# Optimization experiments

Hardware: AMD Instinct MI355X
Metric: run time of the kernel (lower is better)

Reference implementation:

```python
import jax, jax.numpy as jnp
import numpy as np

Q = 4096  # num_quantizing
E = 256   # quantizing_dim


def setup_inputs() -> dict:
    key = jax.random.key(0)
    kx, kw = jax.random.split(key)
    x = jax.random.normal(kx, (16, 2048, E), dtype=jnp.float32)
    # nn.init.normal_(weight, mean=0.0, std=0.001)
    weight = 0.001 * jax.random.normal(kw, (Q, E), dtype=jnp.float32)
    return {"x": x, "weight": weight}


def reference(x, weight):
    # x: (*, E), weight: (Q, E)
    input_shape = x.shape
    xf = x.reshape(-1, weight.shape[1])  # (N, E)
    # Squared L2 distance via norm expansion (same argmin as sum(delta^2)):
    x2 = jnp.sum(xf * xf, axis=1, keepdims=True)          # (N, 1)
    w2 = jnp.sum(weight * weight, axis=1)                  # (Q,)
    dist = x2 - 2.0 * (xf @ weight.T) + w2                 # (N, Q)
    q_idx = jnp.argmin(dist, axis=1)                       # (N,)
    q_data = weight[q_idx]                                 # (N, E)
    return q_data.reshape(input_shape), q_idx.reshape(input_shape[:-1])
```

## Files before the change

### kernel.cpp

```cpp
#include <hip/hip_runtime.h>
#include <cfloat>
#include <climits>

constexpr int E  = 256;
constexpr int Qn = 4096;
constexpr float WSCALE = 4096.0f;


typedef _Float16 half8  __attribute__((ext_vector_type(8)));
typedef _Float16 half4v __attribute__((ext_vector_type(4)));
typedef float    f32x16 __attribute__((ext_vector_type(16)));

#define GAS __attribute__((address_space(1)))
#define LAS __attribute__((address_space(3)))

#define NEG_INF __int_as_float(0xFF800000)

__device__ inline bool lexlt(float a, int ai, float b, int bi) {
    return a < b || (a == b && ai < bi);
}

__global__ __launch_bounds__(256) void prep_kernel(
    const float* __restrict__ x, const float* __restrict__ w,
    _Float16* __restrict__ A16, _Float16* __restrict__ B16,
    float* __restrict__ w2, int nxblocks)
{
    int blk  = blockIdx.x;
    int sub  = threadIdx.x >> 6;
    int lane = threadIdx.x & 63;
    bool isX = blk < nxblocks;
    int row  = (isX ? blk : blk - nxblocks) * 4 + sub;

    const float* src = isX ? x : w;
    float4 v = *(const float4*)(src + (size_t)row * E + lane * 4);

    if (!isX) {
        float s = v.x * v.x + v.y * v.y + v.z * v.z + v.w * v.w;
        #pragma unroll
        for (int off = 32; off; off >>= 1) s += __shfl_xor(s, off);
        if (lane == 0) w2[row] = s;
    }

    float sc = isX ? 1.0f : WSCALE;
    half4v h = { (_Float16)(v.x * sc), (_Float16)(v.y * sc),
                 (_Float16)(v.z * sc), (_Float16)(v.w * sc) };
    _Float16* dst16 = (isX ? A16 : B16) + (size_t)row * 256;
    *(half4v*)(dst16 + lane * 4) = h;
}

__device__ inline void ins4max(float K[4], float k) {
    #pragma unroll
    for (int t = 0; t < 4; ++t) {
        float mx = fmaxf(K[t], k);
        k = fminf(K[t], k);
        K[t] = mx;
    }
}

union SmemU {
    struct { _Float16 W[128 * 64]; _Float16 X[128 * 64]; } st;
    float2 mergeS[128 * 4];
};

__global__ __launch_bounds__(256, 4) void vq_mfma_kernel(
    const _Float16* __restrict__ A16,
    const _Float16* __restrict__ B16,
    float4* __restrict__ top4)
{
    __shared__ SmemU sm;

    const int tid  = threadIdx.x;
    const int w    = tid >> 6;
    const int lane = tid & 63;
    const int l31  = lane & 31;
    const int lh   = lane >> 5;
    const int rb   = blockIdx.x;
    const int cg   = blockIdx.y;

    const int wr = (w & 1) * 64;
    const int wc = (w >> 1) * 64;

    f32x16 acc[2][2];
    #pragma unroll
    for (int f = 0; f < 2; ++f)
        #pragma unroll
        for (int g = 0; g < 2; ++g)
            #pragma unroll
            for (int r = 0; r < 16; ++r) acc[f][g][r] = 0.0f;

    const _Float16* Ab16 = A16 + (size_t)rb * 128 * 256;
    const _Float16* Bb16 = B16 + (size_t)cg * 128 * 256;

    const int srow = lane >> 3;
    const int schk = lane & 7;

    for (int kt = 0; kt < 4; ++kt) {
        __syncthreads();
        #pragma unroll
        for (int inst = 0; inst < 4; ++inst) {
            int drow = w * 32 + inst * 8 + srow;
            int gchk = schk ^ (drow & 7);
            const _Float16* gW = Bb16 + (size_t)drow * 256 + kt * 64 + gchk * 8;
            const _Float16* gX = Ab16 + (size_t)drow * 256 + kt * 64 + gchk * 8;
            __builtin_amdgcn_global_load_lds((const GAS void*)gW,
                (LAS void*)(sm.st.W + w * 2048 + inst * 512), 16, 0, 0);
            __builtin_amdgcn_global_load_lds((const GAS void*)gX,
                (LAS void*)(sm.st.X + w * 2048 + inst * 512), 16, 0, 0);
        }
        __syncthreads();

        #pragma unroll
        for (int s = 0; s < 4; ++s) {
            const int kc = 2 * s + lh;
            half8 wf[2], xf[2];
            #pragma unroll
            for (int f = 0; f < 2; ++f) {
                int fr = wc + 32 * f + l31;
                wf[f] = *(const half8*)(sm.st.W + fr * 64 + ((kc ^ (fr & 7)) << 3));
                int xr = wr + 32 * f + l31;
                xf[f] = *(const half8*)(sm.st.X + xr * 64 + ((kc ^ (xr & 7)) << 3));
            }
            #pragma unroll
            for (int f = 0; f < 2; ++f)
                #pragma unroll
                for (int g = 0; g < 2; ++g)
                    acc[f][g] = __builtin_amdgcn_mfma_f32_32x32x16_f16(
                        wf[f], xf[g], acc[f][g], 0, 0, 0);
        }
    }

    float t1[2] = { NEG_INF, NEG_INF }, t2[2] = { NEG_INF, NEG_INF };

    #pragma unroll
    for (int f = 0; f < 2; ++f)
        #pragma unroll
        for (int r = 0; r < 16; ++r) {
            int m  = (r & 3) + 8 * (r >> 2) + 4 * lh;
            int qg = cg * 128 + wc + 32 * f + m;
            #pragma unroll
            for (int g = 0; g < 2; ++g) {
                float pk = __int_as_float(
                    (__float_as_int(acc[f][g][r]) & 0xFFFFF000) | qg);
                t2[g] = __builtin_amdgcn_fmed3f(t1[g], t2[g], pk);
                t1[g] = fmaxf(t1[g], pk);
            }
        }

    __syncthreads();

    #pragma unroll
    for (int g = 0; g < 2; ++g) {
        int rrow = wr + 32 * g + l31;
        sm.mergeS[rrow * 4 + ((w >> 1) * 2 + lh)] = make_float2(t1[g], t2[g]);
    }
    __syncthreads();

    if (tid < 128) {
        float K[4] = { NEG_INF, NEG_INF, NEG_INF, NEG_INF };
        #pragma unroll
        for (int sl = 0; sl < 4; ++sl) {
            float2 a = sm.mergeS[tid * 4 + sl];
            ins4max(K, a.x);
            ins4max(K, a.y);
        }
        top4[(size_t)(rb * 128 + tid) * 32 + cg] =
            make_float4(K[0], K[1], K[2], K[3]);
    }
}

__global__ __launch_bounds__(256) void finalize_kernel(
    const float4* __restrict__ top4, const float* __restrict__ x,
    const float* __restrict__ w, const float* __restrict__ w2,
    float* __restrict__ qdata, float* __restrict__ qidx)
{
    int row  = blockIdx.x * 4 + (threadIdx.x >> 6);
    int lane = threadIdx.x & 63;

    float cand[4];
    if (lane < 32) {
        float4 c4 = top4[(size_t)row * 32 + lane];
        cand[0] = c4.x; cand[1] = c4.y; cand[2] = c4.z; cand[3] = c4.w;
    } else {
        cand[0] = cand[1] = cand[2] = cand[3] = NEG_INF;
    }

    int chosen[4];
    #pragma unroll
    for (int p = 0; p < 4; ++p) {
        float cur = fmaxf(fmaxf(cand[0], cand[1]), fmaxf(cand[2], cand[3]));
        #pragma unroll
        for (int off = 32; off; off >>= 1)
            cur = fmaxf(cur, __shfl_xor(cur, off));
        int curb = __float_as_int(cur);
        chosen[p] = curb & 0xFFF;
        #pragma unroll
        for (int j = 0; j < 4; ++j)
            if (__float_as_int(cand[j]) == curb) cand[j] = NEG_INF;
    }

    float4 xv = *(const float4*)(x + (size_t)row * E + lane * 4);
    float s2 = xv.x * xv.x + xv.y * xv.y + xv.z * xv.z + xv.w * xv.w;
    float d[4];
    #pragma unroll
    for (int j = 0; j < 4; ++j) {
        float4 wv = *(const float4*)(w + (size_t)chosen[j] * E + lane * 4);
        d[j] = xv.x * wv.x + xv.y * wv.y + xv.z * wv.z + xv.w * wv.w;
    }
    #pragma unroll
    for (int off = 32; off; off >>= 1) {
        s2 += __shfl_xor(s2, off);
        #pragma unroll
        for (int j = 0; j < 4; ++j) d[j] += __shfl_xor(d[j], off);
    }

    float bs = FLT_MAX; int win = INT_MAX;
    #pragma unroll
    for (int j = 0; j < 4; ++j) {
        float s = (s2 - 2.0f * d[j]) + w2[chosen[j]];
        if (lexlt(s, chosen[j], bs, win)) { bs = s; win = chosen[j]; }
    }

    if (lane == 0) qidx[row] = (float)win;
    *(float4*)(qdata + (size_t)row * E + lane * 4) =
        *(const float4*)(w + (size_t)win * E + lane * 4);
}

constexpr int FBM = 64, FBN = 128, FBK = 64, FPAD = 4, FTH = 256;

__global__ __launch_bounds__(64) void row_sumsq_kernel(const float* __restrict__ src,
                                                       float* __restrict__ dst) {
    int row = blockIdx.x, lane = threadIdx.x;
    float4 v = ((const float4*)(src + (size_t)row * E))[lane];
    float s = v.x * v.x + v.y * v.y + v.z * v.z + v.w * v.w;
    #pragma unroll
    for (int off = 32; off > 0; off >>= 1) s += __shfl_down(s, off);
    if (lane == 0) dst[row] = s;
}

__global__ __launch_bounds__(FTH) void vq_fallback_kernel(
    const float* __restrict__ x, const float* __restrict__ w,
    const float* __restrict__ x2, const float* __restrict__ w2,
    float* __restrict__ qdata, float* __restrict__ qidx)
{
    __shared__ float xs[FBM][FBK + FPAD];
    __shared__ float ws[FBN][FBK + FPAD];
    __shared__ float redS[FBM][16];
    __shared__ int   redC[FBM][16];
    __shared__ int   bestC[FBM];

    const int tid = threadIdx.x, tr = tid >> 4, tc = tid & 15;
    const int r0 = blockIdx.x * FBM;
    float best[4]; int bidx[4];
    #pragma unroll
    for (int i = 0; i < 4; ++i) { best[i] = FLT_MAX; bidx[i] = 0x7FFFFFFF; }
    float x2r[4];
    #pragma unroll
    for (int i = 0; i < 4; ++i) x2r[i] = x2[r0 + tr + 16 * i];

    for (int qt = 0; qt < Qn / FBN; ++qt) {
        const int c0 = qt * FBN;
        float acc[4][8];
        #pragma unroll
        for (int i = 0; i < 4; ++i)
            #pragma unroll
            for (int j = 0; j < 8; ++j) acc[i][j] = 0.f;
        for (int kt = 0; kt < E / FBK; ++kt) {
            __syncthreads();
            const int kk = (tid & 15) * 4, rr = tid >> 4;
            #pragma unroll
            for (int m = 0; m < 4; ++m)
                *(float4*)&xs[m * 16 + rr][kk] =
                    *(const float4*)(x + (size_t)(r0 + m * 16 + rr) * E + kt * FBK + kk);
            #pragma unroll
            for (int m = 0; m < 8; ++m)
                *(float4*)&ws[m * 16 + rr][kk] =
                    *(const float4*)(w + (size_t)(c0 + m * 16 + rr) * E + kt * FBK + kk);
            __syncthreads();
            #pragma unroll
            for (int k4 = 0; k4 < FBK / 4; ++k4) {
                float4 a[4], bb[8];
                #pragma unroll
                for (int i = 0; i < 4; ++i) a[i] = *(const float4*)&xs[tr + 16 * i][k4 * 4];
                #pragma unroll
                for (int j = 0; j < 8; ++j) bb[j] = *(const float4*)&ws[tc + 16 * j][k4 * 4];
                #pragma unroll
                for (int i = 0; i < 4; ++i)
                    #pragma unroll
                    for (int j = 0; j < 8; ++j) {
                        acc[i][j] += a[i].x * bb[j].x; acc[i][j] += a[i].y * bb[j].y;
                        acc[i][j] += a[i].z * bb[j].z; acc[i][j] += a[i].w * bb[j].w;
                    }
            }
        }
        #pragma unroll
        for (int i = 0; i < 4; ++i)
            #pragma unroll
            for (int j = 0; j < 8; ++j) {
                int c = c0 + tc + 16 * j;
                float s = (x2r[i] - 2.0f * acc[i][j]) + w2[c];
                if (s < best[i]) { best[i] = s; bidx[i] = c; }
            }
    }
    #pragma unroll
    for (int i = 0; i < 4; ++i) { redS[tr + 16 * i][tc] = best[i]; redC[tr + 16 * i][tc] = bidx[i]; }
    __syncthreads();
    if (tid < FBM) {
        float bs = FLT_MAX; int bc = 0x7FFFFFFF;
        #pragma unroll
        for (int t = 0; t < 16; ++t) {
            float s = redS[tid][t]; int c = redC[tid][t];
            if (s < bs || (s == bs && c < bc)) { bs = s; bc = c; }
        }
        qidx[r0 + tid] = (float)bc; bestC[tid] = bc;
    }
    __syncthreads();
    for (int it = 0; it < FBM / 4; ++it) {
        int row = it * 4 + (tid >> 6), c = bestC[row], kk = (tid & 63) * 4;
        *(float4*)(qdata + (size_t)(r0 + row) * E + kk) = *(const float4*)(w + (size_t)c * E + kk);
    }
}

extern "C" void kernel_launch(void* const* d_in, const int* in_sizes, int n_in,
                              void* d_out, int out_size, void* d_ws, size_t ws_size,
                              hipStream_t stream) {
    const float* x = (const float*)d_in[0];
    const float* w = (const float*)d_in[1];
    const int N = in_sizes[0] / E;

    float* qdata = (float*)d_out;
    float* qidx  = (float*)d_out + (size_t)N * E;

    size_t off = 0;
    auto carve = [&](size_t bytes) { size_t p = off; off += (bytes + 255) & ~(size_t)255; return p; };
    size_t oA16 = carve((size_t)N  * 256 * sizeof(_Float16));
    size_t oB16 = carve((size_t)Qn * 256 * sizeof(_Float16));
    size_t ow2  = carve((size_t)Qn * sizeof(float));
    size_t oT   = carve((size_t)N * 32 * sizeof(float4));
    size_t ox2f = carve((size_t)N * sizeof(float));

    if (ws_size >= off && (N % 128) == 0) {
        char* ws = (char*)d_ws;
        _Float16* A16 = (_Float16*)(ws + oA16);
        _Float16* B16 = (_Float16*)(ws + oB16);
        float* w2    = (float*)(ws + ow2);
        float4* top4 = (float4*)(ws + oT);

        prep_kernel<<<N / 4 + Qn / 4, 256, 0, stream>>>(x, w, A16, B16, w2, N / 4);
        vq_mfma_kernel<<<dim3(N / 128, Qn / 128), 256, 0, stream>>>(A16, B16, top4);
        finalize_kernel<<<N / 4, 256, 0, stream>>>(top4, x, w, w2, qdata, qidx);
    } else {
        float* x2 = (float*)d_ws;
        float* w2 = x2 + N;
        row_sumsq_kernel<<<N, 64, 0, stream>>>(x, x2);
        row_sumsq_kernel<<<Qn, 64, 0, stream>>>(w, w2);
        vq_fallback_kernel<<<N / FBM, FTH, 0, stream>>>(x, w, x2, w2, qdata, qidx);
    }
}
```

Baseline: 198.2 us.

## Enlarge MFMA tile to 256x256 with double-buffered LDS staging

Each workgroup of the distance/top-k kernel now covers 256 input rows by 256 codewords instead of 128x128. It uses 8 waves, each accumulating a 128x64 sub-tile, and swaps the grid order. K-chunk loads are double-buffered in LDS, so the next chunk is fetched while the current one feeds the MFMAs, and wave priority is raised during compute. The aim is more operand reuse per LDS byte and overlap of global loads with matrix math. The cost is much larger LDS use and 128 accumulator registers per lane, which lowers resident waves per CU. It also requires N to be a multiple of 256.

```diff
diff --git a/kernel.cpp b/kernel.cpp
--- a/kernel.cpp
+++ b/kernel.cpp
@@ -58,11 +58,11 @@
 }
 
 union SmemU {
-    struct { _Float16 W[128 * 64]; _Float16 X[128 * 64]; } st;
-    float2 mergeS[128 * 4];
+    struct { _Float16 W[256 * 64]; _Float16 X[256 * 64]; } st[2];
+    float2 mergeS[256 * 2 * 4];
 };
 
-__global__ __launch_bounds__(256, 4) void vq_mfma_kernel(
+__global__ __launch_bounds__(512, 2) void vq_mfma_kernel(
     const _Float16* __restrict__ A16,
     const _Float16* __restrict__ B16,
     float4* __restrict__ top4)
@@ -74,28 +74,27 @@
     const int lane = tid & 63;
     const int l31  = lane & 31;
     const int lh   = lane >> 5;
-    const int rb   = blockIdx.x;
-    const int cg   = blockIdx.y;
-
-    const int wr = (w & 1) * 64;
-    const int wc = (w >> 1) * 64;
-
-    f32x16 acc[2][2];
-    #pragma unroll
-    for (int f = 0; f < 2; ++f)
-        #pragma unroll
-        for (int g = 0; g < 2; ++g)
-            #pragma unroll
-            for (int r = 0; r < 16; ++r) acc[f][g][r] = 0.0f;
-
-    const _Float16* Ab16 = A16 + (size_t)rb * 128 * 256;
-    const _Float16* Bb16 = B16 + (size_t)cg * 128 * 256;
+    const int cwg  = blockIdx.x;
+    const int rb   = blockIdx.y;
+
+    const int wm = w & 1;
+    const int wn = w >> 1;
+
+    f32x16 acc[4][2];
+    #pragma unroll
+    for (int m = 0; m < 4; ++m)
+        #pragma unroll
+        for (int n = 0; n < 2; ++n)
+            #pragma unroll
+            for (int r = 0; r < 16; ++r) acc[m][n][r] = 0.0f;
+
+    const _Float16* Ab16 = A16 + (size_t)rb  * 256 * 256;
+    const _Float16* Bb16 = B16 + (size_t)cwg * 256 * 256;
 
     const int srow = lane >> 3;
     const int schk = lane & 7;
 
-    for (int kt = 0; kt < 4; ++kt) {
-        __syncthreads();
+    auto stage = [&](int kt, int b) {
         #pragma unroll
         for (int inst = 0; inst < 4; ++inst) {
             int drow = w * 32 + inst * 8 + srow;
@@ -103,67 +102,92 @@
             const _Float16* gW = Bb16 + (size_t)drow * 256 + kt * 64 + gchk * 8;
             const _Float16* gX = Ab16 + (size_t)drow * 256 + kt * 64 + gchk * 8;
             __builtin_amdgcn_global_load_lds((const GAS void*)gW,
-                (LAS void*)(sm.st.W + w * 2048 + inst * 512), 16, 0, 0);
+                (LAS void*)(sm.st[b].W + w * 2048 + inst * 512), 16, 0, 0);
             __builtin_amdgcn_global_load_lds((const GAS void*)gX,
-                (LAS void*)(sm.st.X + w * 2048 + inst * 512), 16, 0, 0);
-        }
-        __syncthreads();
-
+                (LAS void*)(sm.st[b].X + w * 2048 + inst * 512), 16, 0, 0);
+        }
+    };
+
+    stage(0, 0);
+    __syncthreads();
+
+    #pragma unroll
+    for (int kt = 0; kt < 4; ++kt) {
+        const int b = kt & 1;
+        if (kt < 3) stage(kt + 1, b ^ 1);
+
+        const _Float16* Wb = sm.st[b].W;
+        const _Float16* Xb = sm.st[b].X;
+
+        __builtin_amdgcn_s_setprio(1);
         #pragma unroll
         for (int s = 0; s < 4; ++s) {
             const int kc = 2 * s + lh;
-            half8 wf[2], xf[2];
-            #pragma unroll
-            for (int f = 0; f < 2; ++f) {
-                int fr = wc + 32 * f + l31;
-                wf[f] = *(const half8*)(sm.st.W + fr * 64 + ((kc ^ (fr & 7)) << 3));
-                int xr = wr + 32 * f + l31;
-                xf[f] = *(const half8*)(sm.st.X + xr * 64 + ((kc ^ (xr & 7)) << 3));
-            }
-            #pragma unroll
-            for (int f = 0; f < 2; ++f)
+            half8 wf[4], xf[2];
+            #pragma unroll
+            for (int m = 0; m < 4; ++m) {
+                int fr = wm * 128 + m * 32 + l31;
+                wf[m] = *(const half8*)(Wb + fr * 64 + ((kc ^ (fr & 7)) << 3));
+            }
+            #pragma unroll
+            for (int n = 0; n < 2; ++n) {
+                int xr = wn * 64 + n * 32 + l31;
+                xf[n] = *(const half8*)(Xb + xr * 64 + ((kc ^ (xr & 7)) << 3));
+            }
+            #pragma unroll
+            for (int m = 0; m < 4; ++m)
                 #pragma unroll
-                for (int g = 0; g < 2; ++g)
-                    acc[f][g] = __builtin_amdgcn_mfma_f32_32x32x16_f16(
-                        wf[f], xf[g], acc[f][g], 0, 0, 0);
-        }
-    }
-
-    float t1[2] = { NEG_INF, NEG_INF }, t2[2] = { NEG_INF, NEG_INF };
-
-    #pragma unroll
-    for (int f = 0; f < 2; ++f)
+                for (int n = 0; n < 2; ++n)
+                    acc[m][n] = __builtin_amdgcn_mfma_f32_32x32x16_f16(
+                        wf[m], xf[n], acc[m][n], 0, 0, 0);
+        }
+        __builtin_amdgcn_s_setprio(0);
+        __syncthreads();
+    }
+
+    float t1[2][2], t2[2][2];
+    #pragma unroll
+    for (int g2 = 0; g2 < 2; ++g2)
+        #pragma unroll
+        for (int n = 0; n < 2; ++n) { t1[g2][n] = NEG_INF; t2[g2][n] = NEG_INF; }
+
+    #pragma unroll
+    for (int m = 0; m < 4; ++m) {
+        const int g2 = m >> 1;
         #pragma unroll
         for (int r = 0; r < 16; ++r) {
-            int m  = (r & 3) + 8 * (r >> 2) + 4 * lh;
-            int qg = cg * 128 + wc + 32 * f + m;
-            #pragma unroll
-            for (int g = 0; g < 2; ++g) {
+            int crow = (r & 3) + 8 * (r >> 2) + 4 * lh;
+            int qg   = cwg * 256 + wm * 128 + m * 32 + crow;
+            #pragma unroll
+            for (int n = 0; n < 2; ++n) {
                 float pk = __int_as_float(
-                    (__float_as_int(acc[f][g][r]) & 0xFFFFF000) | qg);
-                t2[g] = __builtin_amdgcn_fmed3f(t1[g], t2[g], pk);
-                t1[g] = fmaxf(t1[g], pk);
-            }
-        }
-
+                    (__float_as_int(acc[m][n][r]) & 0xFFFFF000) | qg);
+                t2[g2][n] = __builtin_amdgcn_fmed3f(t1[g2][n], t2[g2][n], pk);
+                t1[g2][n] = fmaxf(t1[g2][n], pk);
+            }
+        }
+    }
+
+    #pragma unroll
+    for (int n = 0; n < 2; ++n) {
+        int xrow = wn * 64 + n * 32 + l31;
+        #pragma unroll
+        for (int g2 = 0; g2 < 2; ++g2)
+            sm.mergeS[(xrow * 2 + wm) * 4 + (lh * 2 + g2)] =
+                make_float2(t1[g2][n], t2[g2][n]);
+    }
     __syncthreads();
 
-    #pragma unroll
-    for (int g = 0; g < 2; ++g) {
-        int rrow = wr + 32 * g + l31;
-        sm.mergeS[rrow * 4 + ((w >> 1) * 2 + lh)] = make_float2(t1[g], t2[g]);
-    }
-    __syncthreads();
-
-    if (tid < 128) {
+    {
+        int xrow = tid >> 1, cgl = tid & 1;
         float K[4] = { NEG_INF, NEG_INF, NEG_INF, NEG_INF };
         #pragma unroll
         for (int sl = 0; sl < 4; ++sl) {
-            float2 a = sm.mergeS[tid * 4 + sl];
+            float2 a = sm.mergeS[(xrow * 2 + cgl) * 4 + sl];
             ins4max(K, a.x);
             ins4max(K, a.y);
         }
-        top4[(size_t)(rb * 128 + tid) * 32 + cg] =
+        top4[(size_t)(rb * 256 + xrow) * 32 + cwg * 2 + cgl] =
             make_float4(K[0], K[1], K[2], K[3]);
     }
 }
@@ -338,7 +362,7 @@
     size_t oT   = carve((size_t)N * 32 * sizeof(float4));
     size_t ox2f = carve((size_t)N * sizeof(float));
 
-    if (ws_size >= off && (N % 128) == 0) {
+    if (ws_size >= off && (N % 256) == 0) {
         char* ws = (char*)d_ws;
         _Float16* A16 = (_Float16*)(ws + oA16);
         _Float16* B16 = (_Float16*)(ws + oB16);
@@ -346,7 +370,7 @@
         float4* top4 = (float4*)(ws + oT);
 
         prep_kernel<<<N / 4 + Qn / 4, 256, 0, stream>>>(x, w, A16, B16, w2, N / 4);
-        vq_mfma_kernel<<<dim3(N / 128, Qn / 128), 256, 0, stream>>>(A16, B16, top4);
+        vq_mfma_kernel<<<dim3(Qn / 256, N / 256), 512, 0, stream>>>(A16, B16, top4);
         finalize_kernel<<<N / 4, 256, 0, stream>>>(top4, x, w, w2, qdata, qidx);
     } else {
         float* x2 = (float*)d_ws;
```

Measured after the change: 199.7 us. Within noise of the previous version (+0.7%).

## Make each block sweep the whole codebook with register-resident X and double-buffered W

Applied to the files above, without the earlier changes.

The GEMM kernel now gives each 512-thread block one 128-row tile of X and loops over all 32 codebook tiles. The X fragments are held in registers and W tiles are double-buffered in LDS through async global-to-LDS loads. Top-4 candidates are merged inside the block, so only one float4 per row is written and finalize no longer reduces 32 partial results. This removes the 32x grid over codebook groups and most of the top4 traffic, but it leaves far fewer blocks (256) to fill the GPU and raises register pressure.

```diff
diff --git a/kernel.cpp b/kernel.cpp
--- a/kernel.cpp
+++ b/kernel.cpp
@@ -58,11 +58,11 @@
 }
 
 union SmemU {
-    struct { _Float16 W[128 * 64]; _Float16 X[128 * 64]; } st;
-    float2 mergeS[128 * 4];
+    _Float16 buf[2][4][128][64];
+    float2 mergeS[128 * 16];
 };
 
-__global__ __launch_bounds__(256, 4) void vq_mfma_kernel(
+__global__ __launch_bounds__(512, 2) void vq_mfma_kernel(
     const _Float16* __restrict__ A16,
     const _Float16* __restrict__ B16,
     float4* __restrict__ top4)
@@ -70,101 +70,135 @@
     __shared__ SmemU sm;
 
     const int tid  = threadIdx.x;
-    const int w    = tid >> 6;
+    const int wv   = tid >> 6;
     const int lane = tid & 63;
     const int l31  = lane & 31;
     const int lh   = lane >> 5;
     const int rb   = blockIdx.x;
-    const int cg   = blockIdx.y;
-
-    const int wr = (w & 1) * 64;
-    const int wc = (w >> 1) * 64;
-
-    f32x16 acc[2][2];
-    #pragma unroll
-    for (int f = 0; f < 2; ++f)
-        #pragma unroll
-        for (int g = 0; g < 2; ++g)
-            #pragma unroll
-            for (int r = 0; r < 16; ++r) acc[f][g][r] = 0.0f;
+
+    const int cwg = wv & 3;
+    const int rg  = wv >> 2;
 
     const _Float16* Ab16 = A16 + (size_t)rb * 128 * 256;
-    const _Float16* Bb16 = B16 + (size_t)cg * 128 * 256;
-
-    const int srow = lane >> 3;
-    const int schk = lane & 7;
-
-    for (int kt = 0; kt < 4; ++kt) {
-        __syncthreads();
-        #pragma unroll
-        for (int inst = 0; inst < 4; ++inst) {
-            int drow = w * 32 + inst * 8 + srow;
-            int gchk = schk ^ (drow & 7);
-            const _Float16* gW = Bb16 + (size_t)drow * 256 + kt * 64 + gchk * 8;
-            const _Float16* gX = Ab16 + (size_t)drow * 256 + kt * 64 + gchk * 8;
-            __builtin_amdgcn_global_load_lds((const GAS void*)gW,
-                (LAS void*)(sm.st.W + w * 2048 + inst * 512), 16, 0, 0);
-            __builtin_amdgcn_global_load_lds((const GAS void*)gX,
-                (LAS void*)(sm.st.X + w * 2048 + inst * 512), 16, 0, 0);
-        }
-        __syncthreads();
-
-        #pragma unroll
-        for (int s = 0; s < 4; ++s) {
-            const int kc = 2 * s + lh;
-            half8 wf[2], xf[2];
-            #pragma unroll
-            for (int f = 0; f < 2; ++f) {
-                int fr = wc + 32 * f + l31;
-                wf[f] = *(const half8*)(sm.st.W + fr * 64 + ((kc ^ (fr & 7)) << 3));
-                int xr = wr + 32 * f + l31;
-                xf[f] = *(const half8*)(sm.st.X + xr * 64 + ((kc ^ (xr & 7)) << 3));
-            }
-            #pragma unroll
-            for (int f = 0; f < 2; ++f)
+
+    auto stage128 = [&](const _Float16* src, int bi) {
+        #pragma unroll
+        for (int kt = 0; kt < 4; ++kt)
+            #pragma unroll
+            for (int i = 0; i < 2; ++i) {
+                int row  = i * 64 + wv * 8 + (lane >> 3);
+                int gchk = (lane & 7) ^ (row & 7);
+                const _Float16* g = src + (size_t)row * 256 + kt * 64 + gchk * 8;
+                __builtin_amdgcn_global_load_lds((const GAS void*)g,
+                    (LAS void*)(&sm.buf[bi][kt][i * 64 + wv * 8][0]), 16, 0, 0);
+            }
+    };
+
+    stage128(Ab16, 0);
+    stage128(B16, 1);
+    __syncthreads();
+
+    half8 xf[2][4][4];
+    #pragma unroll
+    for (int n = 0; n < 2; ++n)
+        #pragma unroll
+        for (int kt = 0; kt < 4; ++kt)
+            #pragma unroll
+            for (int s = 0; s < 4; ++s) {
+                int xr = rg * 64 + n * 32 + l31;
+                int kc = 2 * s + lh;
+                xf[n][kt][s] = *(const half8*)(&sm.buf[0][kt][0][0]
+                                + xr * 64 + ((kc ^ (xr & 7)) << 3));
+            }
+    __syncthreads();
+
+    float t1[2][4], t2[2][4];
+    #pragma unroll
+    for (int n = 0; n < 2; ++n)
+        #pragma unroll
+        for (int q = 0; q < 4; ++q) { t1[n][q] = NEG_INF; t2[n][q] = NEG_INF; }
+
+    const int fr = cwg * 32 + l31;
+    const int frsw = fr & 7;
+
+    #pragma unroll
+    for (int q = 0; q < 4; ++q) {
+        for (int tt = 0; tt < 8; ++tt) {
+            const int t  = q * 8 + tt;
+            const int bi = (t + 1) & 1;
+
+            if (t + 1 < 32)
+                stage128(B16 + (size_t)(t + 1) * 128 * 256, t & 1);
+
+            const _Float16* Wb = &sm.buf[bi][0][0][0];
+
+            f32x16 acc0 = {}, acc1 = {};
+            __builtin_amdgcn_s_setprio(1);
+            #pragma unroll
+            for (int kt = 0; kt < 4; ++kt)
                 #pragma unroll
-                for (int g = 0; g < 2; ++g)
-                    acc[f][g] = __builtin_amdgcn_mfma_f32_32x32x16_f16(
-                        wf[f], xf[g], acc[f][g], 0, 0, 0);
-        }
-    }
-
-    float t1[2] = { NEG_INF, NEG_INF }, t2[2] = { NEG_INF, NEG_INF };
-
-    #pragma unroll
-    for (int f = 0; f < 2; ++f)
-        #pragma unroll
-        for (int r = 0; r < 16; ++r) {
-            int m  = (r & 3) + 8 * (r >> 2) + 4 * lh;
-            int qg = cg * 128 + wc + 32 * f + m;
-            #pragma unroll
-            for (int g = 0; g < 2; ++g) {
-                float pk = __int_as_float(
-                    (__float_as_int(acc[f][g][r]) & 0xFFFFF000) | qg);
-                t2[g] = __builtin_amdgcn_fmed3f(t1[g], t2[g], pk);
-                t1[g] = fmaxf(t1[g], pk);
-            }
-        }
-
-    __syncthreads();
-
-    #pragma unroll
-    for (int g = 0; g < 2; ++g) {
-        int rrow = wr + 32 * g + l31;
-        sm.mergeS[rrow * 4 + ((w >> 1) * 2 + lh)] = make_float2(t1[g], t2[g]);
+                for (int s = 0; s < 4; ++s) {
+                    int kc = 2 * s + lh;
+                    half8 wf = *(const half8*)(Wb + kt * 8192
+                                  + fr * 64 + ((kc ^ frsw) << 3));
+                    acc0 = __builtin_amdgcn_mfma_f32_32x32x16_f16(
+                               wf, xf[0][kt][s], acc0, 0, 0, 0);
+                    acc1 = __builtin_amdgcn_mfma_f32_32x32x16_f16(
+                               wf, xf[1][kt][s], acc1, 0, 0, 0);
+                }
+            __builtin_amdgcn_s_setprio(0);
+
+            #pragma unroll
+            for (int r = 0; r < 16; ++r) {
+                int crow = (r & 3) + 8 * (r >> 2) + 4 * lh;
+                int qg   = t * 128 + cwg * 32 + crow;
+                float pk0 = __int_as_float(
+                    (__float_as_int(acc0[r]) & 0xFFFFF000) | qg);
+                t2[0][q] = __builtin_amdgcn_fmed3f(t1[0][q], t2[0][q], pk0);
+                t1[0][q] = fmaxf(t1[0][q], pk0);
+                float pk1 = __int_as_float(
+                    (__float_as_int(acc1[r]) & 0xFFFFF000) | qg);
+                t2[1][q] = __builtin_amdgcn_fmed3f(t1[1][q], t2[1][q], pk1);
+                t1[1][q] = fmaxf(t1[1][q], pk1);
+            }
+
+            __syncthreads();
+        }
+    }
+
+    #pragma unroll
+    for (int n = 0; n < 2; ++n)
+        #pragma unroll
+        for (int q = 0; q < 4; ++q) {
+            float o1 = __shfl_xor(t1[n][q], 32);
+            float o2 = __shfl_xor(t2[n][q], 32);
+            float m1 = fmaxf(t1[n][q], o1);
+            float m2 = __builtin_amdgcn_fmed3f(t1[n][q], o1,
+                                               fmaxf(t2[n][q], o2));
+            t1[n][q] = m1; t2[n][q] = m2;
+        }
+
+    if (lh == 0) {
+        #pragma unroll
+        for (int n = 0; n < 2; ++n) {
+            int row = rg * 64 + n * 32 + l31;
+            #pragma unroll
+            for (int q = 0; q < 4; ++q)
+                sm.mergeS[row * 16 + cwg * 4 + q] =
+                    make_float2(t1[n][q], t2[n][q]);
+        }
     }
     __syncthreads();
 
     if (tid < 128) {
         float K[4] = { NEG_INF, NEG_INF, NEG_INF, NEG_INF };
         #pragma unroll
-        for (int sl = 0; sl < 4; ++sl) {
-            float2 a = sm.mergeS[tid * 4 + sl];
+        for (int sl = 0; sl < 16; ++sl) {
+            float2 a = sm.mergeS[tid * 16 + sl];
             ins4max(K, a.x);
             ins4max(K, a.y);
         }
-        top4[(size_t)(rb * 128 + tid) * 32 + cg] =
-            make_float4(K[0], K[1], K[2], K[3]);
+        top4[(size_t)rb * 128 + tid] = make_float4(K[0], K[1], K[2], K[3]);
     }
 }
 
@@ -176,27 +210,11 @@
     int row  = blockIdx.x * 4 + (threadIdx.x >> 6);
     int lane = threadIdx.x & 63;
 
-    float cand[4];
-    if (lane < 32) {
-        float4 c4 = top4[(size_t)row * 32 + lane];
-        cand[0] = c4.x; cand[1] = c4.y; cand[2] = c4.z; cand[3] = c4.w;
-    } else {
-        cand[0] = cand[1] = cand[2] = cand[3] = NEG_INF;
-    }
-
-    int chosen[4];
-    #pragma unroll
-    for (int p = 0; p < 4; ++p) {
-        float cur = fmaxf(fmaxf(cand[0], cand[1]), fmaxf(cand[2], cand[3]));
-        #pragma unroll
-        for (int off = 32; off; off >>= 1)
-            cur = fmaxf(cur, __shfl_xor(cur, off));
-        int curb = __float_as_int(cur);
-        chosen[p] = curb & 0xFFF;
-        #pragma unroll
-        for (int j = 0; j < 4; ++j)
-            if (__float_as_int(cand[j]) == curb) cand[j] = NEG_INF;
-    }
+    float4 c4 = top4[row];
+    int chosen[4] = { __float_as_int(c4.x) & 0xFFF,
+                      __float_as_int(c4.y) & 0xFFF,
+                      __float_as_int(c4.z) & 0xFFF,
+                      __float_as_int(c4.w) & 0xFFF };
 
     float4 xv = *(const float4*)(x + (size_t)row * E + lane * 4);
     float s2 = xv.x * xv.x + xv.y * xv.y + xv.z * xv.z + xv.w * xv.w;
@@ -335,7 +353,7 @@
     size_t oA16 = carve((size_t)N  * 256 * sizeof(_Float16));
     size_t oB16 = carve((size_t)Qn * 256 * sizeof(_Float16));
     size_t ow2  = carve((size_t)Qn * sizeof(float));
-    size_t oT   = carve((size_t)N * 32 * sizeof(float4));
+    size_t oT   = carve((size_t)N * sizeof(float4));
     size_t ox2f = carve((size_t)N * sizeof(float));
 
     if (ws_size >= off && (N % 128) == 0) {
@@ -346,7 +364,7 @@
         float4* top4 = (float4*)(ws + oT);
 
         prep_kernel<<<N / 4 + Qn / 4, 256, 0, stream>>>(x, w, A16, B16, w2, N / 4);
-        vq_mfma_kernel<<<dim3(N / 128, Qn / 128), 256, 0, stream>>>(A16, B16, top4);
+        vq_mfma_kernel<<<N / 128, 512, 0, stream>>>(A16, B16, top4);
         finalize_kernel<<<N / 4, 256, 0, stream>>>(top4, x, w, w2, qdata, qidx);
     } else {
         float* x2 = (float*)d_ws;
```

Result: faster. 178.0 us, median of 3 (-10.2%).
